# Kernel tuning notes

Hardware: AMD Instinct MI355X
Metric: run time of the kernel (lower is better)

The kernel has to match this reference:

```python
import jax, jax.numpy as jnp
import numpy as np

B, N, DIN, DOUT = 1, 8192, 256, 256
EPS = 1e-8

def setup_inputs() -> dict:
    key = jax.random.key(0)
    kA, kX, k1, k2, k3, k4 = jax.random.split(key, 6)
    A = jax.random.uniform(kA, (B, N, N), dtype=jnp.float32)          # dense adjacency [B,N,N]
    X = jax.random.normal(kX, (B, N, DIN), dtype=jnp.float32)          # node features [B,N,Din]
    s1 = 1.0 / np.sqrt(DIN)
    s2 = 1.0 / np.sqrt(DIN + DOUT)
    W_w = jax.random.uniform(k1, (DIN, DOUT), jnp.float32, -s1, s1)
    b_w = jax.random.uniform(k2, (DOUT,), jnp.float32, -s1, s1)
    W_fc = jax.random.uniform(k3, (DIN + DOUT, DOUT), jnp.float32, -s2, s2)
    b_fc = jax.random.uniform(k4, (DOUT,), jnp.float32, -s2, s2)
    return {"A": A, "X": X, "W_w": W_w, "b_w": b_w, "W_fc": W_fc, "b_fc": b_fc}

def reference(A, X, W_w, b_w, W_fc, b_fc):
    # inputs = relu(weight(X))  [B,N,Dout]
    h = jax.nn.relu(jnp.einsum('bnd,de->bne', X, W_w) + b_w)
    # A[...,None] * inputs[:,None] summed over neighbor dim == matmul (avg pooling)
    pooled = jnp.einsum('bij,bjd->bid', A, h)                # [B,N,Dout]
    size = jnp.sum(A, axis=2, keepdims=True) + EPS           # [B,N,1]
    pooled = pooled / size
    cat = jnp.concatenate([X, pooled], axis=-1)              # [B,N,Din+Dout]
    out = jax.nn.relu(jnp.einsum('bnd,de->bne', cat, W_fc) + b_fc) + EPS
    out = out / (jnp.linalg.norm(out) + EPS)                 # global L2 norm over all elements
    return out
```

## Files before the change

### kernel.cpp

```cpp
#include <hip/hip_runtime.h>
#include <hip/hip_bf16.h>
#include <math.h>

typedef __bf16 bf16;
typedef bf16 bf16x8 __attribute__((ext_vector_type(8)));
typedef bf16 bf16x4 __attribute__((ext_vector_type(4)));
typedef float f32x4 __attribute__((ext_vector_type(4)));

#define N_NODES 8192
#define DIN 256
#define DOUT 256
#define KCAT 512
#define EPSF 1e-8f
#define KSPLIT 4
#define KBLK 2048
#define BM 128
#define BK 64
#define NT (KBLK / BK)
#define BUFSZ 49152

__device__ __forceinline__ f32x4 mfma16(bf16x8 a, bf16x8 b, f32x4 c) {
    return __builtin_amdgcn_mfma_f32_16x16x32_bf16(a, b, c, 0, 0, 0);
}

#define WAITVM(N) asm volatile("s_waitcnt vmcnt(" #N ")" ::: "memory")
#define WAITLGKM  asm volatile("s_waitcnt lgkmcnt(0)" ::: "memory")
#define BAR       __builtin_amdgcn_s_barrier()

__global__ __launch_bounds__(256) void k0_prep(const float* __restrict__ Ww,
                                               const float* __restrict__ Wfc,
                                               bf16* __restrict__ WwT,
                                               bf16* __restrict__ WfcT) {
    int tid = blockIdx.x * 256 + threadIdx.x;
    if (tid < 256 * 256) {
        int n = tid >> 8, k = tid & 255;
        WwT[n * 256 + k] = (bf16)Ww[k * 256 + n];
    }
    if (tid < 256 * 512) {
        int n = tid >> 9, k = tid & 511;
        WfcT[n * 512 + k] = (bf16)Wfc[k * 256 + n];
    }
}

__global__ __launch_bounds__(128) void k1_h(const float* __restrict__ X,
                                            const bf16* __restrict__ WwT,
                                            const float* __restrict__ bw,
                                            bf16* __restrict__ hT) {
    const int lane = threadIdx.x & 63;
    const int wid  = threadIdx.x >> 6;
    const int m0   = blockIdx.x * 16;
    const int lrow = lane & 15;
    const int lk8  = (lane >> 4) * 8;

    f32x4 acc[8];
#pragma unroll
    for (int i = 0; i < 8; ++i) acc[i] = {0.f, 0.f, 0.f, 0.f};

#pragma unroll
    for (int ks = 0; ks < DIN; ks += 32) {
        const float* xp = X + (size_t)(m0 + lrow) * DIN + ks + lk8;
        f32x4 x0 = *reinterpret_cast<const f32x4*>(xp);
        f32x4 x1 = *reinterpret_cast<const f32x4*>(xp + 4);
        bf16x8 a;
#pragma unroll
        for (int j = 0; j < 4; ++j) { a[j] = (bf16)x0[j]; a[4 + j] = (bf16)x1[j]; }
#pragma unroll
        for (int nb = 0; nb < 8; ++nb) {
            int col = wid * 128 + nb * 16 + lrow;
            bf16x8 b = *reinterpret_cast<const bf16x8*>(WwT + (size_t)col * DIN + ks + lk8);
            acc[nb] = mfma16(a, b, acc[nb]);
        }
    }
    const int mrow = m0 + (lane >> 4) * 4;
#pragma unroll
    for (int nb = 0; nb < 8; ++nb) {
        int col = wid * 128 + nb * 16 + lrow;
        float bias = bw[col];
        bf16x4 hv;
#pragma unroll
        for (int j = 0; j < 4; ++j) {
            float v = acc[nb][j] + bias;
            hv[j] = (bf16)(v > 0.f ? v : 0.f);
        }
        *reinterpret_cast<bf16x4*>(hT + (size_t)col * N_NODES + mrow) = hv;
    }
}

__global__ __launch_bounds__(512) void k2_pool(const float* __restrict__ A,
                                               const bf16* __restrict__ hT,
                                               float* __restrict__ part,
                                               float* __restrict__ rsG) {
    __shared__ __align__(16) unsigned char lds[2][BUFSZ];
    __shared__ float rsp[2][BM];
    const int t    = threadIdx.x;
    const int lane = t & 63;
    const int wid  = t >> 6;
    const int wr   = wid >> 2;
    const int wn   = wid & 3;
    const int lrow = lane & 15;
    const int lk4  = lane >> 4;
    const int mblk = blockIdx.x & 63;
    const int ks   = blockIdx.x >> 6;
    const int m0   = mblk * BM;
    const int kbase = ks * KBLK;

    f32x4 acc[4][4];
    f32x4 sums[4];
#pragma unroll
    for (int i = 0; i < 4; ++i) {
        sums[i] = {0.f, 0.f, 0.f, 0.f};
#pragma unroll
        for (int j = 0; j < 4; ++j) acc[i][j] = {0.f, 0.f, 0.f, 0.f};
    }
    bf16x8 bOne;
#pragma unroll
    for (int j = 0; j < 8; ++j) bOne[j] = (bf16)1.0f;

    const int arow = t >> 2;
    const int aq   = t & 3;
    const float* aSrc = A + (size_t)(m0 + arow) * N_NODES + kbase + aq * 16;
    const int awb0 = arow * 128 + (((aq * 2)     ^ (arow & 7)) << 4);
    const int awb1 = arow * 128 + (((aq * 2 + 1) ^ (arow & 7)) << 4);

    int bcol[4], bseg[4], bldsoff[4];
#pragma unroll
    for (int r = 0; r < 4; ++r) {
        int idx = r * 512 + t;
        bcol[r] = idx >> 3;
        bseg[r] = (idx & 7) ^ (bcol[r] & 7);
        bldsoff[r] = 16384 + (r * 8 + wid) * 1024;
    }

    int aOff[2][4], bOff[2][4];
#pragma unroll
    for (int kki = 0; kki < 2; ++kki) {
        int sA = kki * 4 + lk4;
#pragma unroll
        for (int f = 0; f < 4; ++f) {
            int row = wr * 64 + f * 16 + lrow;
            aOff[kki][f] = row * 128 + ((sA ^ (row & 7)) << 4);
            int col = wn * 64 + f * 16 + lrow;
            bOff[kki][f] = 16384 + col * 128 + ((sA ^ (col & 7)) << 4);
        }
    }

    f32x4 ra0, ra1, ra2, ra3;

#define ALOAD(tile) do {                                                      \
        const float* p_ = aSrc + (size_t)(tile) * BK;                         \
        ra0 = *reinterpret_cast<const f32x4*>(p_);                            \
        ra1 = *reinterpret_cast<const f32x4*>(p_ + 4);                        \
        ra2 = *reinterpret_cast<const f32x4*>(p_ + 8);                        \
        ra3 = *reinterpret_cast<const f32x4*>(p_ + 12);                       \
    } while (0)

#define CVTWRITE(bufidx) do {                                                 \
        bf16x8 w0_, w1_;                                                      \
        _Pragma("unroll")                                                     \
        for (int j = 0; j < 4; ++j) {                                         \
            w0_[j] = (bf16)ra0[j]; w0_[4 + j] = (bf16)ra1[j];                 \
            w1_[j] = (bf16)ra2[j]; w1_[4 + j] = (bf16)ra3[j];                 \
        }                                                                     \
        *reinterpret_cast<bf16x8*>(&lds[bufidx][awb0]) = w0_;                 \
        *reinterpret_cast<bf16x8*>(&lds[bufidx][awb1]) = w1_;                 \
    } while (0)

#define BDMA(tile, bufidx) do {                                               \
        _Pragma("unroll")                                                     \
        for (int r_ = 0; r_ < 4; ++r_) {                                      \
            const bf16* g_ = hT + (size_t)bcol[r_] * N_NODES + kbase          \
                             + (tile) * BK + bseg[r_] * 8;                    \
            __builtin_amdgcn_global_load_lds(                                 \
                (const __attribute__((address_space(1))) void*)g_,            \
                (__attribute__((address_space(3))) void*)&lds[bufidx][bldsoff[r_]], \
                16, 0, 0);                                                    \
        }                                                                     \
    } while (0)

#define COMPUTE(bufidx) do {                                                  \
        _Pragma("unroll")                                                     \
        for (int kki = 0; kki < 2; ++kki) {                                   \
            bf16x8 af_[4], bf_[4];                                            \
            _Pragma("unroll")                                                 \
            for (int f = 0; f < 4; ++f) {                                     \
                af_[f] = *reinterpret_cast<const bf16x8*>(&lds[bufidx][aOff[kki][f]]); \
                bf_[f] = *reinterpret_cast<const bf16x8*>(&lds[bufidx][bOff[kki][f]]); \
            }                                                                 \
            _Pragma("unroll")                                                 \
            for (int mf = 0; mf < 4; ++mf)                                    \
                _Pragma("unroll")                                             \
                for (int nf = 0; nf < 4; ++nf)                                \
                    acc[mf][nf] = mfma16(af_[mf], bf_[nf], acc[mf][nf]);      \
            if (wn == kki) {                                                  \
                _Pragma("unroll")                                             \
                for (int mf = 0; mf < 4; ++mf)                                \
                    sums[mf] = mfma16(af_[mf], bOne, sums[mf]);               \
            }                                                                 \
        }                                                                     \
    } while (0)

    ALOAD(0); BDMA(0, 0);
    CVTWRITE(0);
    ALOAD(1); BDMA(1, 1);
    WAITVM(8);
    WAITLGKM;
    BAR;

    for (int tt = 0; tt < NT - 2; ++tt) {
        CVTWRITE((tt + 1) & 1);
        COMPUTE(tt & 1);
        ALOAD(tt + 2);
        WAITVM(4);
        WAITLGKM;
        BAR;
        BDMA(tt + 2, tt & 1);
    }
    CVTWRITE((NT - 1) & 1);
    COMPUTE((NT - 2) & 1);
    WAITVM(0);
    WAITLGKM;
    BAR;
    COMPUTE((NT - 1) & 1);

    if (wn < 2 && lrow == 0) {
#pragma unroll
        for (int mf = 0; mf < 4; ++mf)
#pragma unroll
            for (int j = 0; j < 4; ++j)
                rsp[wn][wr * 64 + mf * 16 + lk4 * 4 + j] = sums[mf][j];
    }
    __syncthreads();
    if (t < BM) rsG[(size_t)ks * N_NODES + m0 + t] = rsp[0][t] + rsp[1][t];

    float* pp = part + ((size_t)ks * N_NODES + m0) * DOUT;
#pragma unroll
    for (int mf = 0; mf < 4; ++mf)
#pragma unroll
        for (int nf = 0; nf < 4; ++nf) {
            int col = wn * 64 + nf * 16 + lrow;
#pragma unroll
            for (int j = 0; j < 4; ++j) {
                int row = wr * 64 + mf * 16 + lk4 * 4 + j;
                pp[(size_t)row * DOUT + col] = acc[mf][nf][j];
            }
        }
#undef ALOAD
#undef CVTWRITE
#undef BDMA
#undef COMPUTE
}

__global__ __launch_bounds__(256) void k2b_combine(const float* __restrict__ part,
                                                   const float* __restrict__ rsG,
                                                   bf16* __restrict__ pooled) {
    int fl  = blockIdx.x * 256 + threadIdx.x;
    int row = fl >> 6;
    int c4  = (fl & 63) * 4;
    f32x4 s = {0.f, 0.f, 0.f, 0.f};
#pragma unroll
    for (int ks = 0; ks < KSPLIT; ++ks) {
        f32x4 v = *reinterpret_cast<const f32x4*>(part + ((size_t)ks * N_NODES + row) * DOUT + c4);
#pragma unroll
        for (int j = 0; j < 4; ++j) s[j] += v[j];
    }
    float rs = EPSF;
#pragma unroll
    for (int ks = 0; ks < KSPLIT; ++ks) rs += rsG[(size_t)ks * N_NODES + row];
    float inv = 1.f / rs;
    bf16x4 o;
#pragma unroll
    for (int j = 0; j < 4; ++j) o[j] = (bf16)(s[j] * inv);
    *reinterpret_cast<bf16x4*>(pooled + (size_t)row * DOUT + c4) = o;
}

__global__ __launch_bounds__(128) void k3_out(const float* __restrict__ X,
                                              const bf16* __restrict__ pooled,
                                              const bf16* __restrict__ WfcT,
                                              const float* __restrict__ bfc,
                                              float* __restrict__ out,
                                              float* __restrict__ partials) {
    const int lane = threadIdx.x & 63;
    const int wid  = threadIdx.x >> 6;
    const int m0   = blockIdx.x * 16;
    const int lrow = lane & 15;
    const int lk8  = (lane >> 4) * 8;

    f32x4 acc[8];
#pragma unroll
    for (int i = 0; i < 8; ++i) acc[i] = {0.f, 0.f, 0.f, 0.f};

#pragma unroll
    for (int ks = 0; ks < 256; ks += 32) {
        const float* xp = X + (size_t)(m0 + lrow) * DIN + ks + lk8;
        f32x4 x0 = *reinterpret_cast<const f32x4*>(xp);
        f32x4 x1 = *reinterpret_cast<const f32x4*>(xp + 4);
        bf16x8 a;
#pragma unroll
        for (int j = 0; j < 4; ++j) { a[j] = (bf16)x0[j]; a[4 + j] = (bf16)x1[j]; }
#pragma unroll
        for (int nb = 0; nb < 8; ++nb) {
            int col = wid * 128 + nb * 16 + lrow;
            bf16x8 b = *reinterpret_cast<const bf16x8*>(WfcT + (size_t)col * KCAT + ks + lk8);
            acc[nb] = mfma16(a, b, acc[nb]);
        }
    }
#pragma unroll
    for (int ks = 256; ks < 512; ks += 32) {
        bf16x8 a = *reinterpret_cast<const bf16x8*>(pooled + (size_t)(m0 + lrow) * DOUT + (ks - 256) + lk8);
#pragma unroll
        for (int nb = 0; nb < 8; ++nb) {
            int col = wid * 128 + nb * 16 + lrow;
            bf16x8 b = *reinterpret_cast<const bf16x8*>(WfcT + (size_t)col * KCAT + ks + lk8);
            acc[nb] = mfma16(a, b, acc[nb]);
        }
    }

    float ss = 0.f;
#pragma unroll
    for (int nb = 0; nb < 8; ++nb) {
        int col = wid * 128 + nb * 16 + lrow;
        float bias = bfc[col];
#pragma unroll
        for (int j = 0; j < 4; ++j) {
            int row = m0 + (lane >> 4) * 4 + j;
            float v = acc[nb][j] + bias;
            v = (v > 0.f ? v : 0.f) + EPSF;
            out[(size_t)row * DOUT + col] = v;
            ss += v * v;
        }
    }
#pragma unroll
    for (int off = 32; off; off >>= 1) ss += __shfl_xor(ss, off);
    __shared__ float sw[2];
    if (lane == 0) sw[wid] = ss;
    __syncthreads();
    if (threadIdx.x == 0) partials[blockIdx.x] = sw[0] + sw[1];
}

__global__ __launch_bounds__(256) void k4_norm(float* __restrict__ out,
                                               const float* __restrict__ partials) {
    __shared__ float sw[4];
    float s = partials[threadIdx.x] + partials[threadIdx.x + 256];
#pragma unroll
    for (int off = 32; off; off >>= 1) s += __shfl_xor(s, off);
    if ((threadIdx.x & 63) == 0) sw[threadIdx.x >> 6] = s;
    __syncthreads();
    float total = sw[0] + sw[1] + sw[2] + sw[3];
    float scale = 1.f / (sqrtf(total) + EPSF);
    f32x4* o4 = reinterpret_cast<f32x4*>(out);
    const int nvec = N_NODES * DOUT / 4;
    for (int i = blockIdx.x * blockDim.x + threadIdx.x; i < nvec; i += gridDim.x * blockDim.x) {
        f32x4 v = o4[i];
#pragma unroll
        for (int j = 0; j < 4; ++j) v[j] *= scale;
        o4[i] = v;
    }
}

extern "C" void kernel_launch(void* const* d_in, const int* in_sizes, int n_in,
                              void* d_out, int out_size, void* d_ws, size_t ws_size,
                              hipStream_t stream) {
    const float* A   = (const float*)d_in[0];
    const float* X   = (const float*)d_in[1];
    const float* Ww  = (const float*)d_in[2];
    const float* bw  = (const float*)d_in[3];
    const float* Wfc = (const float*)d_in[4];
    const float* bfc = (const float*)d_in[5];
    float* out = (float*)d_out;

    char* ws = (char*)d_ws;
    bf16*  hT        = (bf16*)(ws);
    bf16*  pooled    = (bf16*)(ws + (4u << 20));
    bf16*  WwT       = (bf16*)(ws + (8u << 20));
    bf16*  WfcT      = (bf16*)(ws + (8u << 20) + (128u << 10));
    float* partials  = (float*)(ws + (8u << 20) + (384u << 10));
    float* rsG       = (float*)(ws + (8u << 20) + (512u << 10));
    float* part      = (float*)(ws + (16u << 20));

    k0_prep<<<512, 256, 0, stream>>>(Ww, Wfc, WwT, WfcT);
    k1_h<<<512, 128, 0, stream>>>(X, WwT, bw, hT);
    k2_pool<<<256, 512, 0, stream>>>(A, hT, part, rsG);
    k2b_combine<<<N_NODES * DOUT / 1024, 256, 0, stream>>>(part, rsG, pooled);
    k3_out<<<512, 128, 0, stream>>>(X, pooled, WfcT, bfc, out, partials);
    k4_norm<<<256, 256, 0, stream>>>(out, partials);
}
```

Measured before the change: 138.0 us.

## Shrink pooling GEMM tiles to BM=64, BK=32 and double block count

The pooling kernel's tile changes from 128x256 rows with K-step 64 to 64x256 rows with K-step 32. LDS per block drops from about 96KB to about 40KB and launch bounds now request 4 blocks per CU, so the grid grows from 256 to 512 blocks. The LDS swizzles, DMA mapping, wait counts and row-sum distribution across warps are reworked to match. The aim is better occupancy and load balance over the 256 CUs while streaming A, at the cost of reading hT twice as often and doing fewer MFMAs per barrier.

New measurement: 162.3 us. 17.6% more time.

```diff
diff --git a/kernel.cpp b/kernel.cpp
--- a/kernel.cpp
+++ b/kernel.cpp
@@ -14,10 +14,11 @@
 #define EPSF 1e-8f
 #define KSPLIT 4
 #define KBLK 2048
-#define BM 128
-#define BK 64
+#define BM 64
+#define BK 32
 #define NT (KBLK / BK)
-#define BUFSZ 49152
+#define BBASE 4096
+#define BUFSZ 20480
 
 __device__ __forceinline__ f32x4 mfma16(bf16x8 a, bf16x8 b, f32x4 c) {
     return __builtin_amdgcn_mfma_f32_16x16x32_bf16(a, b, c, 0, 0, 0);
@@ -86,12 +87,12 @@
     }
 }
 
-__global__ __launch_bounds__(512) void k2_pool(const float* __restrict__ A,
-                                               const bf16* __restrict__ hT,
-                                               float* __restrict__ part,
-                                               float* __restrict__ rsG) {
+__global__ __launch_bounds__(512, 4) void k2_pool(const float* __restrict__ A,
+                                                  const bf16* __restrict__ hT,
+                                                  float* __restrict__ part,
+                                                  float* __restrict__ rsG) {
     __shared__ __align__(16) unsigned char lds[2][BUFSZ];
-    __shared__ float rsp[2][BM];
+    __shared__ float rsp[4][BM];
     const int t    = threadIdx.x;
     const int lane = t & 63;
     const int wid  = t >> 6;
@@ -99,15 +100,15 @@
     const int wn   = wid & 3;
     const int lrow = lane & 15;
     const int lk4  = lane >> 4;
-    const int mblk = blockIdx.x & 63;
-    const int ks   = blockIdx.x >> 6;
+    const int mblk = blockIdx.x & 127;
+    const int ks   = blockIdx.x >> 7;
     const int m0   = mblk * BM;
     const int kbase = ks * KBLK;
 
-    f32x4 acc[4][4];
-    f32x4 sums[4];
-#pragma unroll
-    for (int i = 0; i < 4; ++i) {
+    f32x4 acc[2][4];
+    f32x4 sums[2];
+#pragma unroll
+    for (int i = 0; i < 2; ++i) {
         sums[i] = {0.f, 0.f, 0.f, 0.f};
 #pragma unroll
         for (int j = 0; j < 4; ++j) acc[i][j] = {0.f, 0.f, 0.f, 0.f};
@@ -116,131 +117,117 @@
 #pragma unroll
     for (int j = 0; j < 8; ++j) bOne[j] = (bf16)1.0f;
 
-    const int arow = t >> 2;
-    const int aq   = t & 3;
-    const float* aSrc = A + (size_t)(m0 + arow) * N_NODES + kbase + aq * 16;
-    const int awb0 = arow * 128 + (((aq * 2)     ^ (arow & 7)) << 4);
-    const int awb1 = arow * 128 + (((aq * 2 + 1) ^ (arow & 7)) << 4);
-
-    int bcol[4], bseg[4], bldsoff[4];
-#pragma unroll
-    for (int r = 0; r < 4; ++r) {
+    const int arow = t >> 3;
+    const int apos = t & 7;
+    const float* aSrc = A + (size_t)(m0 + arow) * N_NODES + kbase + apos * 4;
+    const int awb = arow * 64 + ((((apos >> 1) ^ ((arow >> 1) & 3))) << 4) + (apos & 1) * 8;
+
+    const bf16* bsrc[2];
+    int bdst[2];
+#pragma unroll
+    for (int r = 0; r < 2; ++r) {
         int idx = r * 512 + t;
-        bcol[r] = idx >> 3;
-        bseg[r] = (idx & 7) ^ (bcol[r] & 7);
-        bldsoff[r] = 16384 + (r * 8 + wid) * 1024;
-    }
-
-    int aOff[2][4], bOff[2][4];
-#pragma unroll
-    for (int kki = 0; kki < 2; ++kki) {
-        int sA = kki * 4 + lk4;
-#pragma unroll
-        for (int f = 0; f < 4; ++f) {
-            int row = wr * 64 + f * 16 + lrow;
-            aOff[kki][f] = row * 128 + ((sA ^ (row & 7)) << 4);
-            int col = wn * 64 + f * 16 + lrow;
-            bOff[kki][f] = 16384 + col * 128 + ((sA ^ (col & 7)) << 4);
-        }
-    }
-
-    f32x4 ra0, ra1, ra2, ra3;
-
-#define ALOAD(tile) do {                                                      \
-        const float* p_ = aSrc + (size_t)(tile) * BK;                         \
-        ra0 = *reinterpret_cast<const f32x4*>(p_);                            \
-        ra1 = *reinterpret_cast<const f32x4*>(p_ + 4);                        \
-        ra2 = *reinterpret_cast<const f32x4*>(p_ + 8);                        \
-        ra3 = *reinterpret_cast<const f32x4*>(p_ + 12);                       \
+        int col = idx >> 2;
+        int gs  = (idx & 3) ^ ((col >> 1) & 3);
+        bsrc[r] = hT + (size_t)col * N_NODES + kbase + gs * 8;
+        bdst[r] = BBASE + r * 8192 + wid * 1024;
+    }
+
+    int aOff[2], bOff[4];
+#pragma unroll
+    for (int mf = 0; mf < 2; ++mf) {
+        int row = wr * 32 + mf * 16 + lrow;
+        aOff[mf] = row * 64 + ((lk4 ^ ((row >> 1) & 3)) << 4);
+    }
+#pragma unroll
+    for (int nf = 0; nf < 4; ++nf) {
+        int col = wn * 64 + nf * 16 + lrow;
+        bOff[nf] = BBASE + col * 64 + ((lk4 ^ ((col >> 1) & 3)) << 4);
+    }
+
+    f32x4 ra;
+
+#define ALOAD(tile) do { ra = *reinterpret_cast<const f32x4*>(aSrc + (size_t)(tile) * BK); } while (0)
+
+#define CVTWRITE(bufidx) do {                                                 \
+        bf16x4 w_;                                                            \
+        _Pragma("unroll")                                                     \
+        for (int j = 0; j < 4; ++j) w_[j] = (bf16)ra[j];                      \
+        *reinterpret_cast<bf16x4*>(&lds[bufidx][awb]) = w_;                   \
     } while (0)
 
-#define CVTWRITE(bufidx) do {                                                 \
-        bf16x8 w0_, w1_;                                                      \
-        _Pragma("unroll")                                                     \
-        for (int j = 0; j < 4; ++j) {                                         \
-            w0_[j] = (bf16)ra0[j]; w0_[4 + j] = (bf16)ra1[j];                 \
-            w1_[j] = (bf16)ra2[j]; w1_[4 + j] = (bf16)ra3[j];                 \
-        }                                                                     \
-        *reinterpret_cast<bf16x8*>(&lds[bufidx][awb0]) = w0_;                 \
-        *reinterpret_cast<bf16x8*>(&lds[bufidx][awb1]) = w1_;                 \
-    } while (0)
-
 #define BDMA(tile, bufidx) do {                                               \
         _Pragma("unroll")                                                     \
-        for (int r_ = 0; r_ < 4; ++r_) {                                      \
-            const bf16* g_ = hT + (size_t)bcol[r_] * N_NODES + kbase          \
-                             + (tile) * BK + bseg[r_] * 8;                    \
+        for (int r_ = 0; r_ < 2; ++r_) {                                      \
             __builtin_amdgcn_global_load_lds(                                 \
-                (const __attribute__((address_space(1))) void*)g_,            \
-                (__attribute__((address_space(3))) void*)&lds[bufidx][bldsoff[r_]], \
+                (const __attribute__((address_space(1))) void*)(bsrc[r_] + (size_t)(tile) * BK), \
+                (__attribute__((address_space(3))) void*)&lds[bufidx][bdst[r_]], \
                 16, 0, 0);                                                    \
         }                                                                     \
     } while (0)
 
-#define COMPUTE(bufidx) do {                                                  \
-        _Pragma("unroll")                                                     \
-        for (int kki = 0; kki < 2; ++kki) {                                   \
-            bf16x8 af_[4], bf_[4];                                            \
+#define COMPUTE(bufidx, tile) do {                                            \
+        bf16x8 af_[2], bf_[4];                                                \
+        _Pragma("unroll")                                                     \
+        for (int f = 0; f < 2; ++f)                                           \
+            af_[f] = *reinterpret_cast<const bf16x8*>(&lds[bufidx][aOff[f]]); \
+        _Pragma("unroll")                                                     \
+        for (int f = 0; f < 4; ++f)                                           \
+            bf_[f] = *reinterpret_cast<const bf16x8*>(&lds[bufidx][bOff[f]]); \
+        _Pragma("unroll")                                                     \
+        for (int mf = 0; mf < 2; ++mf)                                        \
             _Pragma("unroll")                                                 \
-            for (int f = 0; f < 4; ++f) {                                     \
-                af_[f] = *reinterpret_cast<const bf16x8*>(&lds[bufidx][aOff[kki][f]]); \
-                bf_[f] = *reinterpret_cast<const bf16x8*>(&lds[bufidx][bOff[kki][f]]); \
-            }                                                                 \
-            _Pragma("unroll")                                                 \
-            for (int mf = 0; mf < 4; ++mf)                                    \
-                _Pragma("unroll")                                             \
-                for (int nf = 0; nf < 4; ++nf)                                \
-                    acc[mf][nf] = mfma16(af_[mf], bf_[nf], acc[mf][nf]);      \
-            if (wn == kki) {                                                  \
-                _Pragma("unroll")                                             \
-                for (int mf = 0; mf < 4; ++mf)                                \
-                    sums[mf] = mfma16(af_[mf], bOne, sums[mf]);               \
-            }                                                                 \
+            for (int nf = 0; nf < 4; ++nf)                                    \
+                acc[mf][nf] = mfma16(af_[mf], bf_[nf], acc[mf][nf]);          \
+        if (wn == ((tile) & 3)) {                                             \
+            sums[0] = mfma16(af_[0], bOne, sums[0]);                          \
+            sums[1] = mfma16(af_[1], bOne, sums[1]);                          \
         }                                                                     \
     } while (0)
 
     ALOAD(0); BDMA(0, 0);
     CVTWRITE(0);
     ALOAD(1); BDMA(1, 1);
-    WAITVM(8);
+    WAITVM(3);
     WAITLGKM;
     BAR;
 
     for (int tt = 0; tt < NT - 2; ++tt) {
         CVTWRITE((tt + 1) & 1);
-        COMPUTE(tt & 1);
+        COMPUTE(tt & 1, tt);
         ALOAD(tt + 2);
-        WAITVM(4);
+        WAITVM(1);
         WAITLGKM;
         BAR;
         BDMA(tt + 2, tt & 1);
     }
     CVTWRITE((NT - 1) & 1);
-    COMPUTE((NT - 2) & 1);
+    COMPUTE((NT - 2) & 1, NT - 2);
     WAITVM(0);
     WAITLGKM;
     BAR;
-    COMPUTE((NT - 1) & 1);
-
-    if (wn < 2 && lrow == 0) {
-#pragma unroll
-        for (int mf = 0; mf < 4; ++mf)
+    COMPUTE((NT - 1) & 1, NT - 1);
+
+    if (lrow == 0) {
+#pragma unroll
+        for (int mf = 0; mf < 2; ++mf)
 #pragma unroll
             for (int j = 0; j < 4; ++j)
-                rsp[wn][wr * 64 + mf * 16 + lk4 * 4 + j] = sums[mf][j];
+                rsp[wn][wr * 32 + mf * 16 + lk4 * 4 + j] = sums[mf][j];
     }
     __syncthreads();
-    if (t < BM) rsG[(size_t)ks * N_NODES + m0 + t] = rsp[0][t] + rsp[1][t];
+    if (t < BM)
+        rsG[(size_t)ks * N_NODES + m0 + t] = rsp[0][t] + rsp[1][t] + rsp[2][t] + rsp[3][t];
 
     float* pp = part + ((size_t)ks * N_NODES + m0) * DOUT;
 #pragma unroll
-    for (int mf = 0; mf < 4; ++mf)
+    for (int mf = 0; mf < 2; ++mf)
 #pragma unroll
         for (int nf = 0; nf < 4; ++nf) {
             int col = wn * 64 + nf * 16 + lrow;
 #pragma unroll
             for (int j = 0; j < 4; ++j) {
-                int row = wr * 64 + mf * 16 + lk4 * 4 + j;
+                int row = wr * 32 + mf * 16 + lk4 * 4 + j;
                 pp[(size_t)row * DOUT + col] = acc[mf][nf][j];
             }
         }
@@ -379,7 +366,7 @@
 
     k0_prep<<<512, 256, 0, stream>>>(Ww, Wfc, WwT, WfcT);
     k1_h<<<512, 128, 0, stream>>>(X, WwT, bw, hT);
-    k2_pool<<<256, 512, 0, stream>>>(A, hT, part, rsG);
+    k2_pool<<<512, 512, 0, stream>>>(A, hT, part, rsG);
     k2b_combine<<<N_NODES * DOUT / 1024, 256, 0, stream>>>(part, rsG, pooled);
     k3_out<<<512, 128, 0, stream>>>(X, pooled, WfcT, bfc, out, partials);
     k4_norm<<<256, 256, 0, stream>>>(out, partials);
```

## Fuse split-K combine into output GEMM and stagger pooling tile order

Applied to the files above, without the earlier changes.

Removes the separate combine kernel: the output GEMM now reads the four split-K partial sums and row sums directly, normalises, and converts to bf16 in registers before the MFMA. It also rotates the starting K tile per block in the pooling kernel so concurrent blocks hit different address ranges of A and hT. This saves a launch and the pooled round trip, but k3 now reads 4x fp32 partials per row, and each of its blocks repeats that reduction across its waves.

Result: no change. 138.4 us (+0.3%).

```diff
diff --git a/kernel.cpp b/kernel.cpp
--- a/kernel.cpp
+++ b/kernel.cpp
@@ -103,6 +103,9 @@
     const int ks   = blockIdx.x >> 6;
     const int m0   = mblk * BM;
     const int kbase = ks * KBLK;
+    const int start = (5 * mblk + 8 * ks) & (NT - 1);
+
+#define PHYS(tl) (((tl) + start) & (NT - 1))
 
     f32x4 acc[4][4];
     f32x4 sums[4];
@@ -147,7 +150,7 @@
     f32x4 ra0, ra1, ra2, ra3;
 
 #define ALOAD(tile) do {                                                      \
-        const float* p_ = aSrc + (size_t)(tile) * BK;                         \
+        const float* p_ = aSrc + (size_t)PHYS(tile) * BK;                     \
         ra0 = *reinterpret_cast<const f32x4*>(p_);                            \
         ra1 = *reinterpret_cast<const f32x4*>(p_ + 4);                        \
         ra2 = *reinterpret_cast<const f32x4*>(p_ + 8);                        \
@@ -169,7 +172,7 @@
         _Pragma("unroll")                                                     \
         for (int r_ = 0; r_ < 4; ++r_) {                                      \
             const bf16* g_ = hT + (size_t)bcol[r_] * N_NODES + kbase          \
-                             + (tile) * BK + bseg[r_] * 8;                    \
+                             + (size_t)PHYS(tile) * BK + bseg[r_] * 8;        \
             __builtin_amdgcn_global_load_lds(                                 \
                 (const __attribute__((address_space(1))) void*)g_,            \
                 (__attribute__((address_space(3))) void*)&lds[bufidx][bldsoff[r_]], \
@@ -248,33 +251,12 @@
 #undef CVTWRITE
 #undef BDMA
 #undef COMPUTE
-}
-
-__global__ __launch_bounds__(256) void k2b_combine(const float* __restrict__ part,
-                                                   const float* __restrict__ rsG,
-                                                   bf16* __restrict__ pooled) {
-    int fl  = blockIdx.x * 256 + threadIdx.x;
-    int row = fl >> 6;
-    int c4  = (fl & 63) * 4;
-    f32x4 s = {0.f, 0.f, 0.f, 0.f};
-#pragma unroll
-    for (int ks = 0; ks < KSPLIT; ++ks) {
-        f32x4 v = *reinterpret_cast<const f32x4*>(part + ((size_t)ks * N_NODES + row) * DOUT + c4);
-#pragma unroll
-        for (int j = 0; j < 4; ++j) s[j] += v[j];
-    }
-    float rs = EPSF;
-#pragma unroll
-    for (int ks = 0; ks < KSPLIT; ++ks) rs += rsG[(size_t)ks * N_NODES + row];
-    float inv = 1.f / rs;
-    bf16x4 o;
-#pragma unroll
-    for (int j = 0; j < 4; ++j) o[j] = (bf16)(s[j] * inv);
-    *reinterpret_cast<bf16x4*>(pooled + (size_t)row * DOUT + c4) = o;
+#undef PHYS
 }
 
 __global__ __launch_bounds__(128) void k3_out(const float* __restrict__ X,
-                                              const bf16* __restrict__ pooled,
+                                              const float* __restrict__ part,
+                                              const float* __restrict__ rsG,
                                               const bf16* __restrict__ WfcT,
                                               const float* __restrict__ bfc,
                                               float* __restrict__ out,
@@ -289,9 +271,14 @@
 #pragma unroll
     for (int i = 0; i < 8; ++i) acc[i] = {0.f, 0.f, 0.f, 0.f};
 
-#pragma unroll
-    for (int ks = 0; ks < 256; ks += 32) {
-        const float* xp = X + (size_t)(m0 + lrow) * DIN + ks + lk8;
+    float rs = EPSF;
+#pragma unroll
+    for (int sp = 0; sp < KSPLIT; ++sp) rs += rsG[(size_t)sp * N_NODES + m0 + lrow];
+    const float inv = 1.f / rs;
+
+#pragma unroll
+    for (int ksx = 0; ksx < 256; ksx += 32) {
+        const float* xp = X + (size_t)(m0 + lrow) * DIN + ksx + lk8;
         f32x4 x0 = *reinterpret_cast<const f32x4*>(xp);
         f32x4 x1 = *reinterpret_cast<const f32x4*>(xp + 4);
         bf16x8 a;
@@ -300,17 +287,28 @@
 #pragma unroll
         for (int nb = 0; nb < 8; ++nb) {
             int col = wid * 128 + nb * 16 + lrow;
-            bf16x8 b = *reinterpret_cast<const bf16x8*>(WfcT + (size_t)col * KCAT + ks + lk8);
+            bf16x8 b = *reinterpret_cast<const bf16x8*>(WfcT + (size_t)col * KCAT + ksx + lk8);
             acc[nb] = mfma16(a, b, acc[nb]);
         }
     }
 #pragma unroll
-    for (int ks = 256; ks < 512; ks += 32) {
-        bf16x8 a = *reinterpret_cast<const bf16x8*>(pooled + (size_t)(m0 + lrow) * DOUT + (ks - 256) + lk8);
+    for (int ksx = 256; ksx < 512; ksx += 32) {
+        f32x4 s0 = {0.f, 0.f, 0.f, 0.f}, s1 = {0.f, 0.f, 0.f, 0.f};
+#pragma unroll
+        for (int sp = 0; sp < KSPLIT; ++sp) {
+            const float* pp = part + ((size_t)sp * N_NODES + m0 + lrow) * DOUT + (ksx - 256) + lk8;
+            f32x4 v0 = *reinterpret_cast<const f32x4*>(pp);
+            f32x4 v1 = *reinterpret_cast<const f32x4*>(pp + 4);
+#pragma unroll
+            for (int j = 0; j < 4; ++j) { s0[j] += v0[j]; s1[j] += v1[j]; }
+        }
+        bf16x8 a;
+#pragma unroll
+        for (int j = 0; j < 4; ++j) { a[j] = (bf16)(s0[j] * inv); a[4 + j] = (bf16)(s1[j] * inv); }
 #pragma unroll
         for (int nb = 0; nb < 8; ++nb) {
             int col = wid * 128 + nb * 16 + lrow;
-            bf16x8 b = *reinterpret_cast<const bf16x8*>(WfcT + (size_t)col * KCAT + ks + lk8);
+            bf16x8 b = *reinterpret_cast<const bf16x8*>(WfcT + (size_t)col * KCAT + ksx + lk8);
             acc[nb] = mfma16(a, b, acc[nb]);
         }
     }
@@ -370,9 +368,8 @@
 
     char* ws = (char*)d_ws;
     bf16*  hT        = (bf16*)(ws);
-    bf16*  pooled    = (bf16*)(ws + (4u << 20));
     bf16*  WwT       = (bf16*)(ws + (8u << 20));
-    bf16*  WfcT      = (bf16*)(ws + (8u << 20) + (128u << 10));
+    bf16*  WfcT     = (bf16*)(ws + (8u << 20) + (128u << 10));
     float* partials  = (float*)(ws + (8u << 20) + (384u << 10));
     float* rsG       = (float*)(ws + (8u << 20) + (512u << 10));
     float* part      = (float*)(ws + (16u << 20));
@@ -380,7 +377,6 @@
     k0_prep<<<512, 256, 0, stream>>>(Ww, Wfc, WwT, WfcT);
     k1_h<<<512, 128, 0, stream>>>(X, WwT, bw, hT);
     k2_pool<<<256, 512, 0, stream>>>(A, hT, part, rsG);
-    k2b_combine<<<N_NODES * DOUT / 1024, 256, 0, stream>>>(part, rsG, pooled);
-    k3_out<<<512, 128, 0, stream>>>(X, pooled, WfcT, bfc, out, partials);
+    k3_out<<<512, 128, 0, stream>>>(X, part, rsG, WfcT, bfc, out, partials);
     k4_norm<<<256, 256, 0, stream>>>(out, partials);
 }
```
